# Kernel optimization log

Hardware: AMD Instinct MI355X
Metric: run time of the kernel (lower is better)

Reference implementation:

```python
import jax, jax.numpy as jnp
import numpy as np

B, T, D, H = 4, 2048, 1024, 16
HD = D // H  # 64
LOCAL_CTX, BLOCKSIZE, VERTSIZE = 256, 1, 16
STRIDE = LOCAL_CTX // BLOCKSIZE  # 256


def build_fixed_mask(n):
    # num_verts == 1 branch of generate_fixed_attention_mask
    layout = np.zeros((n, n), dtype=np.bool_)
    # vertical stripes: top `vertsize` indices of each stride block
    for idx in range(STRIDE - VERTSIZE, STRIDE):
        layout[:, idx::STRIDE] = True
    rows = np.arange(n)
    # local: each query attends to its own stride-block
    same_block = (rows[:, None] // STRIDE) == (rows[None, :] // STRIDE)
    layout |= same_block
    # causal: zero out k > q
    layout &= rows[None, :] <= rows[:, None]
    return layout


def setup_inputs() -> dict:
    key = jax.random.key(0)
    k1, k2, k3, k4, k5 = jax.random.split(key, 5)
    s = 0.02
    return {
        "x": jax.random.normal(k1, (B, T, D), dtype=jnp.float32),
        "Wqkv": jax.random.normal(k2, (D, 3 * D), dtype=jnp.float32) * s,
        "bqkv": jax.random.normal(k3, (3 * D,), dtype=jnp.float32) * s,
        "Wproj": jax.random.normal(k4, (D, D), dtype=jnp.float32) * s,
        "bproj": jax.random.normal(k5, (D,), dtype=jnp.float32) * s,
        "mask": jnp.asarray(build_fixed_mask(T)),
    }


def reference(x, Wqkv, bqkv, Wproj, bproj, mask):
    b, t, _ = x.shape
    qkv = (x @ Wqkv + bqkv).reshape(b, t, 3, H, HD)
    # (B,T,3,H,HD) -> (B,H,T,HD) per component
    q = qkv[:, :, 0].transpose(0, 2, 1, 3)
    k = qkv[:, :, 1].transpose(0, 2, 1, 3)
    v = qkv[:, :, 2].transpose(0, 2, 1, 3)
    att = jnp.einsum("bhqd,bhkd->bhqk", q, k) * (1.0 / jnp.sqrt(jnp.float32(HD)))
    att = jnp.where(mask[:t, :t], att, -jnp.inf)
    att = jax.nn.softmax(att, axis=-1)
    y = jnp.einsum("bhqk,bhkd->bhqd", att, v)
    y = y.transpose(0, 2, 1, 3).reshape(b, t, D)
    return y @ Wproj + bproj
```

## Files before the change

### kernel.cpp

```cpp
#include <hip/hip_runtime.h>
#include <cstdint>
#include <cstddef>

typedef unsigned short u16;
typedef __attribute__((ext_vector_type(8))) short short8;
typedef __attribute__((ext_vector_type(4))) float f32x4;
typedef __attribute__((ext_vector_type(4))) unsigned short u16x4;

#define B_ 4
#define T_ 2048
#define D_ 1024
#define H_ 16
#define HD_ 64

__device__ __forceinline__ u16 f2bf(float f) {
  union { float f; unsigned i; } v; v.f = f;
  unsigned r = (v.i + 0x7FFFu + ((v.i >> 16) & 1u)) >> 16;
  return (u16)r;
}

__device__ __forceinline__ void load_lds16(const void* g, void* l) {
  __builtin_amdgcn_global_load_lds(
      (const __attribute__((address_space(1))) void*)g,
      (__attribute__((address_space(3))) void*)l, 16, 0, 0);
}

#define BAR() __builtin_amdgcn_s_barrier()
#define VMC(n) asm volatile("s_waitcnt vmcnt(" #n ")" ::: "memory")

__global__ __launch_bounds__(256) void cvt_f32_bf16(const float* __restrict__ src,
                                                    u16* __restrict__ dst) {
  const size_t i = ((size_t)blockIdx.x * 256 + threadIdx.x) * 4;
  const f32x4 v = *(const f32x4*)(src + i);
  u16x4 o;
#pragma unroll
  for (int r = 0; r < 4; ++r) o[r] = f2bf(v[r]);
  *(u16x4*)(dst + i) = o;
}

__global__ __launch_bounds__(256) void transpose_cvt(const float* __restrict__ src,
                                                     u16* __restrict__ dst,
                                                     int R, int C) {
  __shared__ u16 t[32][33];
  const int c0 = blockIdx.x * 32, r0 = blockIdx.y * 32;
  const int tid = threadIdx.x;
  const int lr = tid >> 5, lc = tid & 31;
#pragma unroll
  for (int p = 0; p < 4; ++p)
    t[lr + p * 8][lc] = f2bf(src[(size_t)(r0 + lr + p * 8) * C + c0 + lc]);
  __syncthreads();
#pragma unroll
  for (int p = 0; p < 4; ++p)
    dst[(size_t)(c0 + lr + p * 8) * R + r0 + lc] = t[lc][lr + p * 8];
}

template <int EPI>
__global__ __launch_bounds__(512, 2)
void gemm8p(const u16* __restrict__ A, const u16* __restrict__ Bt,
            const float* __restrict__ bias, int K, int N,
            void* __restrict__ o0v, u16* __restrict__ o1, u16* __restrict__ o2) {
  __shared__ u16 tbuf[65536];
  const int tid = threadIdx.x;
  const int lane = tid & 63;
  const int w = tid >> 6;
  const int q = lane >> 4, col = lane & 15;

  const int nbx = gridDim.x;
  const int id = blockIdx.y * nbx + blockIdx.x;
  const int nwg = nbx * gridDim.y;
  const int sid = (id & 7) * (nwg >> 3) + (id >> 3);
  const int m0 = (sid / nbx) * 256, n0 = (sid % nbx) * 256;

  const int c8 = ((lane & 7) ^ (lane >> 3)) * 8;
  const size_t go0 = (size_t)(w * 16 + (lane >> 3)) * K + c8;
  const size_t go1 = (size_t)(w * 16 + 8 + (lane >> 3)) * K + c8;
  const int d0 = w * 1024 + lane * 8, d1 = d0 + 512;

  auto STAGE = [&](int isB, int buf, int half, int tile) {
    const u16* s = isB ? Bt : A;
    const u16* g = s + (size_t)((isB ? n0 : m0) + half * 128) * K + ((size_t)tile << 6);
    u16* d = tbuf + (isB ? 32768 : 0) + (buf * 2 + half) * 8192;
    load_lds16(g + go0, d + d0);
    load_lds16(g + go1, d + d1);
  };

  short8 af[4][2], bfr[2][2];
  const int arow = (w >> 2) * 64 + col;
  const int brow = (w & 3) * 32 + col;
  const int sA0 = ((0 * 4 + q) ^ (col & 7)) * 8, sA1 = ((1 * 4 + q) ^ (col & 7)) * 8;

  auto LDA = [&](int buf, int pm) {
    const u16* base = tbuf + (buf * 2 + pm) * 8192;
#pragma unroll
    for (int i = 0; i < 4; ++i) {
      af[i][0] = *(const short8*)&base[(arow + i * 16) * 64 + sA0];
      af[i][1] = *(const short8*)&base[(arow + i * 16) * 64 + sA1];
    }
  };
  auto LDB = [&](int buf, int pn) {
    const u16* base = tbuf + 32768 + (buf * 2 + pn) * 8192;
#pragma unroll
    for (int j = 0; j < 2; ++j) {
      bfr[j][0] = *(const short8*)&base[(brow + j * 16) * 64 + sA0];
      bfr[j][1] = *(const short8*)&base[(brow + j * 16) * 64 + sA1];
    }
  };

  f32x4 acc[8][4] = {};
  auto MM = [&](int pm, int pn) {
    __builtin_amdgcn_s_setprio(1);
#pragma unroll
    for (int i = 0; i < 4; ++i)
#pragma unroll
      for (int j = 0; j < 2; ++j) {
        acc[pm * 4 + i][pn * 2 + j] =
            __builtin_amdgcn_mfma_f32_16x16x32_bf16(af[i][0], bfr[j][0], acc[pm * 4 + i][pn * 2 + j], 0, 0, 0);
        acc[pm * 4 + i][pn * 2 + j] =
            __builtin_amdgcn_mfma_f32_16x16x32_bf16(af[i][1], bfr[j][1], acc[pm * 4 + i][pn * 2 + j], 0, 0, 0);
      }
    __builtin_amdgcn_s_setprio(0);
  };

  const int NI = K >> 7;

  STAGE(0, 0, 0, 0); STAGE(0, 0, 1, 0); STAGE(1, 0, 0, 0); STAGE(1, 0, 1, 0);
  STAGE(0, 1, 0, 1); STAGE(0, 1, 1, 1); STAGE(1, 1, 0, 1);
  VMC(0);
  BAR();

  for (int i = 0; i < NI; ++i) {
    const int t1 = 2 * i + 1, t2 = 2 * i + 2, t3 = 2 * i + 3;
    const bool pf = (i < NI - 1);
    LDA(0, 0); LDB(0, 0);
    STAGE(1, 1, 1, t1);
    BAR(); MM(0, 0); BAR();
    LDB(0, 1);
    if (pf) STAGE(0, 0, 0, t2);
    BAR(); MM(0, 1); BAR();
    LDA(0, 1); LDB(0, 0);
    BAR(); MM(1, 0); BAR();
    LDB(0, 1);
    if (pf) { STAGE(1, 0, 0, t2); STAGE(0, 0, 1, t2); }
    BAR(); MM(1, 1);
    if (pf) { VMC(6); } else { VMC(0); }
    BAR();
    LDA(1, 0); LDB(1, 0);
    if (pf) STAGE(1, 0, 1, t2);
    BAR(); MM(0, 0); BAR();
    LDB(1, 1);
    if (pf) STAGE(0, 1, 0, t3);
    BAR(); MM(0, 1); BAR();
    LDA(1, 1); LDB(1, 0);
    BAR(); MM(1, 0); BAR();
    LDB(1, 1);
    if (pf) { STAGE(1, 1, 0, t3); STAGE(0, 1, 1, t3); }
    BAR(); MM(1, 1);
    if (pf) { VMC(6); }
    BAR();
  }

#pragma unroll
  for (int bj = 0; bj < 4; ++bj) {
    const int n = n0 + (w & 3) * 32 + (bj >> 1) * 128 + (bj & 1) * 16 + col;
    const float bv = bias[n];
    if constexpr (EPI == 0) {
      u16* q0p = (u16*)o0v;
      const int c = n >> 10, rem = n & 1023, hh = rem >> 6, dd = rem & 63;
#pragma unroll
      for (int a = 0; a < 8; ++a) {
        const int mrow = m0 + (w >> 2) * 64 + (a >> 2) * 128 + (a & 3) * 16 + q * 4;
        const int b = mrow >> 11, t2r = mrow & 2047;
        const int bh = b * H_ + hh;
        if (c == 0) {
#pragma unroll
          for (int r = 0; r < 4; ++r)
            q0p[((size_t)bh * T_ + t2r + r) * HD_ + dd] = f2bf((acc[a][bj][r] + bv) * 0.125f);
        } else if (c == 1) {
#pragma unroll
          for (int r = 0; r < 4; ++r)
            o1[((size_t)bh * T_ + t2r + r) * HD_ + dd] = f2bf(acc[a][bj][r] + bv);
        } else {
          u16x4 pk;
#pragma unroll
          for (int r = 0; r < 4; ++r) pk[r] = f2bf(acc[a][bj][r] + bv);
          *(u16x4*)&o2[((size_t)bh * HD_ + dd) * T_ + t2r] = pk;
        }
      }
    } else {
      float* outp = (float*)o0v;
#pragma unroll
      for (int a = 0; a < 8; ++a) {
        const int mrow = m0 + (w >> 2) * 64 + (a >> 2) * 128 + (a & 3) * 16 + q * 4;
#pragma unroll
        for (int r = 0; r < 4; ++r)
          outp[(size_t)(mrow + r) * N + n] = acc[a][bj][r] + bv;
      }
    }
  }
}

template <int EPI>
__global__ __launch_bounds__(256)
void gemm_bt(const u16* __restrict__ A, const u16* __restrict__ Bt,
             const float* __restrict__ bias, int K, int N,
             void* __restrict__ o0v, u16* __restrict__ o1, u16* __restrict__ o2) {
  __shared__ u16 As[128 * 32];
  __shared__ u16 Bs[128 * 32];
  const int tid = threadIdx.x;
  const int lane = tid & 63;
  const int w = tid >> 6;
  const int q = lane >> 4, col = lane & 15;
  const int m0 = blockIdx.y * 128, n0 = blockIdx.x * 128;
  const int wm = (w >> 1) * 64, wn = (w & 1) * 64;
  const int srow = tid >> 2, soff = (tid & 3) * 8;

  f32x4 acc[4][4] = {};

  const u16* Ap = A + (size_t)(m0 + srow) * K + soff;
  const u16* Bp = Bt + (size_t)(n0 + srow) * K + soff;

  for (int kb = 0; kb < K; kb += 32) {
    load_lds16(Ap + kb, &As[tid * 8]);
    load_lds16(Ap + (size_t)64 * K + kb, &As[2048 + tid * 8]);
    load_lds16(Bp + kb, &Bs[tid * 8]);
    load_lds16(Bp + (size_t)64 * K + kb, &Bs[2048 + tid * 8]);
    __syncthreads();
    short8 af[4], bfr[4];
#pragma unroll
    for (int i = 0; i < 4; ++i)
      af[i] = *(const short8*)&As[(wm + i * 16 + col) * 32 + q * 8];
#pragma unroll
    for (int j = 0; j < 4; ++j)
      bfr[j] = *(const short8*)&Bs[(wn + j * 16 + col) * 32 + q * 8];
#pragma unroll
    for (int i = 0; i < 4; ++i)
#pragma unroll
      for (int j = 0; j < 4; ++j)
        acc[i][j] = __builtin_amdgcn_mfma_f32_16x16x32_bf16(af[i], bfr[j], acc[i][j], 0, 0, 0);
    __syncthreads();
  }

#pragma unroll
  for (int j = 0; j < 4; ++j) {
    const int n = n0 + wn + j * 16 + col;
    const float bv = bias[n];
    if constexpr (EPI == 0) {
      u16* q0p = (u16*)o0v;
      const int c = n >> 10, rem = n & 1023, hh = rem >> 6, dd = rem & 63;
#pragma unroll
      for (int i = 0; i < 4; ++i) {
        const int mrow = m0 + wm + i * 16 + q * 4;
        const int b = mrow >> 11, t = mrow & 2047;
        const int bh = b * H_ + hh;
        if (c == 0) {
#pragma unroll
          for (int r = 0; r < 4; ++r)
            q0p[((size_t)bh * T_ + t + r) * HD_ + dd] = f2bf((acc[i][j][r] + bv) * 0.125f);
        } else if (c == 1) {
#pragma unroll
          for (int r = 0; r < 4; ++r)
            o1[((size_t)bh * T_ + t + r) * HD_ + dd] = f2bf(acc[i][j][r] + bv);
        } else {
          u16x4 pk;
#pragma unroll
          for (int r = 0; r < 4; ++r) pk[r] = f2bf(acc[i][j][r] + bv);
          *(u16x4*)&o2[((size_t)bh * HD_ + dd) * T_ + t] = pk;
        }
      }
    } else {
      float* outp = (float*)o0v;
#pragma unroll
      for (int i = 0; i < 4; ++i) {
        const int mrow = m0 + wm + i * 16 + q * 4;
#pragma unroll
        for (int r = 0; r < 4; ++r)
          outp[(size_t)(mrow + r) * N + n] = acc[i][j][r] + bv;
      }
    }
  }
}

__global__ __launch_bounds__(256)
void sparse_attn(const u16* __restrict__ Qb, const u16* __restrict__ Kb,
                 const u16* __restrict__ Vt, u16* __restrict__ Y) {
  __shared__ char smem[20480];
  u16* Pall = (u16*)smem;
  float* Obuf = (float*)smem;

  const int tid = threadIdx.x, lane = tid & 63, w = tid >> 6;
  const int q = lane >> 4, col = lane & 15;
  const int bh = blockIdx.x, qt = blockIdx.y;
  const int b = bh >> 4, hh = bh & 15;
  const int qb = qt >> 2;
  const int rb = (qt & 3) * 64;
  const int qg = qt * 64;
  const u16* Qh = Qb + (size_t)bh * T_ * HD_;
  const u16* Kh = Kb + (size_t)bh * T_ * HD_;
  const u16* Vh = Vt + (size_t)bh * HD_ * T_;

  short8 qf[4][2];
#pragma unroll
  for (int i = 0; i < 4; ++i)
#pragma unroll
    for (int h2 = 0; h2 < 2; ++h2)
      qf[i][h2] = *(const short8*)&Qh[(size_t)(qg + i * 16 + col) * HD_ + h2 * 32 + q * 8];

  f32x4 o[4][4] = {};
  f32x4 lI[4] = {};
  const short8 ones = {0x3F80, 0x3F80, 0x3F80, 0x3F80, 0x3F80, 0x3F80, 0x3F80, 0x3F80};

  u16* P = Pall + w * 2560;

  const int ns = (qb + 1) >> 1;
  const int L = ns + 2 * (qt & 3) + 2;

  for (int j = w; j < L; j += 4) {
    int k0, k1, localc;
    bool mask1;
    if (j < ns) {
      k0 = (2 * j) * 256 + 240; k1 = k0 + 256;
      mask1 = (2 * j + 1 == qb); localc = -1;
    } else {
      const int c = j - ns;
      k0 = qb * 256 + c * 32; k1 = k0 + 16;
      mask1 = false; localc = c * 32;
    }
    short8 k0a = *(const short8*)&Kh[(size_t)(k0 + col) * HD_ + q * 8];
    short8 k0b = *(const short8*)&Kh[(size_t)(k0 + col) * HD_ + 32 + q * 8];
    short8 k1a = *(const short8*)&Kh[(size_t)(k1 + col) * HD_ + q * 8];
    short8 k1b = *(const short8*)&Kh[(size_t)(k1 + col) * HD_ + 32 + q * 8];
    const int kvb = (q < 2) ? (k0 + q * 8) : (k1 + (q - 2) * 8);
    short8 vf[4];
#pragma unroll
    for (int dt = 0; dt < 4; ++dt)
      vf[dt] = *(const short8*)&Vh[(size_t)(dt * 16 + col) * T_ + kvb];
#pragma unroll
    for (int rt = 0; rt < 4; ++rt) {
      f32x4 z = {0.f, 0.f, 0.f, 0.f};
      f32x4 s0 = __builtin_amdgcn_mfma_f32_16x16x32_bf16(qf[rt][0], k0a, z, 0, 0, 0);
      s0 = __builtin_amdgcn_mfma_f32_16x16x32_bf16(qf[rt][1], k0b, s0, 0, 0, 0);
      f32x4 s1 = __builtin_amdgcn_mfma_f32_16x16x32_bf16(qf[rt][0], k1a, z, 0, 0, 0);
      s1 = __builtin_amdgcn_mfma_f32_16x16x32_bf16(qf[rt][1], k1b, s1, 0, 0, 0);
#pragma unroll
      for (int r = 0; r < 4; ++r) {
        float p0 = __expf(s0[r]);
        float p1 = mask1 ? 0.f : __expf(s1[r]);
        if (localc >= 0) {
          const int qr = rb + rt * 16 + q * 4 + r;
          if (localc + col > qr) p0 = 0.f;
          if (localc + 16 + col > qr) p1 = 0.f;
        }
        P[(rt * 16 + q * 4 + r) * 40 + col] = f2bf(p0);
        P[(rt * 16 + q * 4 + r) * 40 + 16 + col] = f2bf(p1);
      }
    }
    asm volatile("s_waitcnt lgkmcnt(0)" ::: "memory");
    short8 pf[4];
#pragma unroll
    for (int rt = 0; rt < 4; ++rt)
      pf[rt] = *(const short8*)&P[(rt * 16 + col) * 40 + q * 8];
#pragma unroll
    for (int rt = 0; rt < 4; ++rt) {
#pragma unroll
      for (int dt = 0; dt < 4; ++dt)
        o[rt][dt] = __builtin_amdgcn_mfma_f32_16x16x32_bf16(pf[rt], vf[dt], o[rt][dt], 0, 0, 0);
      lI[rt] = __builtin_amdgcn_mfma_f32_16x16x32_bf16(pf[rt], ones, lI[rt], 0, 0, 0);
    }
  }

#pragma unroll
  for (int rt = 0; rt < 4; ++rt) {
    __syncthreads();
#pragma unroll
    for (int dt = 0; dt < 4; ++dt)
      *(f32x4*)&Obuf[(w * 65 + dt * 16 + col) * 16 + q * 4] = o[rt][dt];
    if (col == 0)
      *(f32x4*)&Obuf[(w * 65 + 64) * 16 + q * 4] = lI[rt];
    __syncthreads();
    f32x4 acc = {0.f, 0.f, 0.f, 0.f};
    f32x4 lt = {0.f, 0.f, 0.f, 0.f};
#pragma unroll
    for (int w2 = 0; w2 < 4; ++w2) {
      acc += *(const f32x4*)&Obuf[(w2 * 65 + w * 16 + col) * 16 + q * 4];
      lt += *(const f32x4*)&Obuf[(w2 * 65 + 64) * 16 + q * 4];
    }
#pragma unroll
    for (int r = 0; r < 4; ++r) {
      const int trow = qg + rt * 16 + q * 4 + r;
      Y[((size_t)(b * T_ + trow)) * D_ + hh * HD_ + w * 16 + col] = f2bf(acc[r] / lt[r]);
    }
  }
}

extern "C" void kernel_launch(void* const* d_in, const int* in_sizes, int n_in,
                              void* d_out, int out_size, void* d_ws, size_t ws_size,
                              hipStream_t stream) {
  const float* x = (const float*)d_in[0];
  const float* Wqkv = (const float*)d_in[1];
  const float* bqkv = (const float*)d_in[2];
  const float* Wproj = (const float*)d_in[3];
  const float* bproj = (const float*)d_in[4];
  float* out = (float*)d_out;

  char* ws = (char*)d_ws;
  u16* xb     = (u16*)(ws + 0);
  u16* WqkvT  = (u16*)(ws + 16777216);
  u16* WprojT = (u16*)(ws + 23068672);
  u16* Qb     = (u16*)(ws + 25165824);
  u16* Kb     = (u16*)(ws + 41943040);
  u16* Vt     = (u16*)(ws + 58720256);
  u16* Y      = (u16*)(ws + 75497472);

  cvt_f32_bf16<<<dim3(8192), 256, 0, stream>>>(x, xb);
  transpose_cvt<<<dim3(96, 32), 256, 0, stream>>>(Wqkv, WqkvT, 1024, 3072);
  transpose_cvt<<<dim3(32, 32), 256, 0, stream>>>(Wproj, WprojT, 1024, 1024);
  gemm8p<0><<<dim3(12, 32), 512, 0, stream>>>(xb, WqkvT, bqkv, 1024, 3072, Qb, Kb, Vt);
  sparse_attn<<<dim3(64, 32), 256, 0, stream>>>(Qb, Kb, Vt, Y);
  gemm_bt<1><<<dim3(8, 64), 256, 0, stream>>>(Y, WprojT, bproj, 1024, 1024, out, nullptr, nullptr);
}
```

Baseline: 258.9 us.

## Merge preprocessing kernels, swizzle proj GEMM tiles, prefetch K fragments in attention

Three unrelated changes. The x conversion and the two weight transposes now run as one launch, removing two kernel launches. The output-projection GEMM remaps workgroup IDs across eight groups to change L2 locality. The sparse attention loop software-prefetches the next iteration's K fragments so their latency overlaps the current MFMA and softmax work, at the cost of more registers.

Measured after the change: 254.7 us. No clear change (-1.6%).

```diff
diff --git a/kernel.cpp b/kernel.cpp
--- a/kernel.cpp
+++ b/kernel.cpp
@@ -28,22 +28,31 @@
 #define BAR() __builtin_amdgcn_s_barrier()
 #define VMC(n) asm volatile("s_waitcnt vmcnt(" #n ")" ::: "memory")
 
-__global__ __launch_bounds__(256) void cvt_f32_bf16(const float* __restrict__ src,
-                                                    u16* __restrict__ dst) {
-  const size_t i = ((size_t)blockIdx.x * 256 + threadIdx.x) * 4;
-  const f32x4 v = *(const f32x4*)(src + i);
-  u16x4 o;
-#pragma unroll
-  for (int r = 0; r < 4; ++r) o[r] = f2bf(v[r]);
-  *(u16x4*)(dst + i) = o;
-}
-
-__global__ __launch_bounds__(256) void transpose_cvt(const float* __restrict__ src,
-                                                     u16* __restrict__ dst,
-                                                     int R, int C) {
+__global__ __launch_bounds__(256)
+void pre_all(const float* __restrict__ x, u16* __restrict__ xb,
+             const float* __restrict__ Wqkv, u16* __restrict__ WqkvT,
+             const float* __restrict__ Wproj, u16* __restrict__ WprojT) {
   __shared__ u16 t[32][33];
-  const int c0 = blockIdx.x * 32, r0 = blockIdx.y * 32;
+  const int bid = blockIdx.x;
   const int tid = threadIdx.x;
+  if (bid < 8192) {
+    const size_t i = ((size_t)bid * 256 + tid) * 4;
+    const f32x4 v = *(const f32x4*)(x + i);
+    u16x4 o;
+#pragma unroll
+    for (int r = 0; r < 4; ++r) o[r] = f2bf(v[r]);
+    *(u16x4*)(xb + i) = o;
+    return;
+  }
+  const float* src; u16* dst; int R, C, bx, by;
+  if (bid < 11264) {
+    const int tb = bid - 8192;
+    bx = tb % 96; by = tb / 96; src = Wqkv; dst = WqkvT; R = 1024; C = 3072;
+  } else {
+    const int tb = bid - 11264;
+    bx = tb & 31; by = tb >> 5; src = Wproj; dst = WprojT; R = 1024; C = 1024;
+  }
+  const int c0 = bx * 32, r0 = by * 32;
   const int lr = tid >> 5, lc = tid & 31;
 #pragma unroll
   for (int p = 0; p < 4; ++p)
@@ -210,7 +219,13 @@
   const int lane = tid & 63;
   const int w = tid >> 6;
   const int q = lane >> 4, col = lane & 15;
-  const int m0 = blockIdx.y * 128, n0 = blockIdx.x * 128;
+
+  const int nbx = gridDim.x;
+  const int id = blockIdx.y * nbx + blockIdx.x;
+  const int nwg = nbx * gridDim.y;
+  const int sid = (id & 7) * (nwg >> 3) + (id >> 3);
+  const int m0 = (sid / nbx) * 128, n0 = (sid % nbx) * 128;
+
   const int wm = (w >> 1) * 64, wn = (w & 1) * 64;
   const int srow = tid >> 2, soff = (tid & 3) * 8;
 
@@ -314,9 +329,7 @@
   const int ns = (qb + 1) >> 1;
   const int L = ns + 2 * (qt & 3) + 2;
 
-  for (int j = w; j < L; j += 4) {
-    int k0, k1, localc;
-    bool mask1;
+  auto params = [&](int j, int& k0, int& k1, bool& mask1, int& localc) {
     if (j < ns) {
       k0 = (2 * j) * 256 + 240; k1 = k0 + 256;
       mask1 = (2 * j + 1 == qb); localc = -1;
@@ -325,22 +338,38 @@
       k0 = qb * 256 + c * 32; k1 = k0 + 16;
       mask1 = false; localc = c * 32;
     }
-    short8 k0a = *(const short8*)&Kh[(size_t)(k0 + col) * HD_ + q * 8];
-    short8 k0b = *(const short8*)&Kh[(size_t)(k0 + col) * HD_ + 32 + q * 8];
-    short8 k1a = *(const short8*)&Kh[(size_t)(k1 + col) * HD_ + q * 8];
-    short8 k1b = *(const short8*)&Kh[(size_t)(k1 + col) * HD_ + 32 + q * 8];
+  };
+  auto ldK = [&](int k0, int k1, short8* kf) {
+    kf[0] = *(const short8*)&Kh[(size_t)(k0 + col) * HD_ + q * 8];
+    kf[1] = *(const short8*)&Kh[(size_t)(k0 + col) * HD_ + 32 + q * 8];
+    kf[2] = *(const short8*)&Kh[(size_t)(k1 + col) * HD_ + q * 8];
+    kf[3] = *(const short8*)&Kh[(size_t)(k1 + col) * HD_ + 32 + q * 8];
+  };
+
+  int k0 = 0, k1 = 0, localc = -1;
+  bool mask1 = false;
+  short8 kf[4];
+  if (w < L) { params(w, k0, k1, mask1, localc); ldK(k0, k1, kf); }
+
+  for (int j = w; j < L; j += 4) {
     const int kvb = (q < 2) ? (k0 + q * 8) : (k1 + (q - 2) * 8);
     short8 vf[4];
 #pragma unroll
     for (int dt = 0; dt < 4; ++dt)
       vf[dt] = *(const short8*)&Vh[(size_t)(dt * 16 + col) * T_ + kvb];
+    int nk0 = 0, nk1 = 0, nlocalc = -1;
+    bool nmask1 = false;
+    short8 nkf[4];
+    const bool hn = (j + 4) < L;
+    if (hn) { params(j + 4, nk0, nk1, nmask1, nlocalc); ldK(nk0, nk1, nkf); }
+
 #pragma unroll
     for (int rt = 0; rt < 4; ++rt) {
       f32x4 z = {0.f, 0.f, 0.f, 0.f};
-      f32x4 s0 = __builtin_amdgcn_mfma_f32_16x16x32_bf16(qf[rt][0], k0a, z, 0, 0, 0);
-      s0 = __builtin_amdgcn_mfma_f32_16x16x32_bf16(qf[rt][1], k0b, s0, 0, 0, 0);
-      f32x4 s1 = __builtin_amdgcn_mfma_f32_16x16x32_bf16(qf[rt][0], k1a, z, 0, 0, 0);
-      s1 = __builtin_amdgcn_mfma_f32_16x16x32_bf16(qf[rt][1], k1b, s1, 0, 0, 0);
+      f32x4 s0 = __builtin_amdgcn_mfma_f32_16x16x32_bf16(qf[rt][0], kf[0], z, 0, 0, 0);
+      s0 = __builtin_amdgcn_mfma_f32_16x16x32_bf16(qf[rt][1], kf[1], s0, 0, 0, 0);
+      f32x4 s1 = __builtin_amdgcn_mfma_f32_16x16x32_bf16(qf[rt][0], kf[2], z, 0, 0, 0);
+      s1 = __builtin_amdgcn_mfma_f32_16x16x32_bf16(qf[rt][1], kf[3], s1, 0, 0, 0);
 #pragma unroll
       for (int r = 0; r < 4; ++r) {
         float p0 = __expf(s0[r]);
@@ -366,6 +395,10 @@
         o[rt][dt] = __builtin_amdgcn_mfma_f32_16x16x32_bf16(pf[rt], vf[dt], o[rt][dt], 0, 0, 0);
       lI[rt] = __builtin_amdgcn_mfma_f32_16x16x32_bf16(pf[rt], ones, lI[rt], 0, 0, 0);
     }
+    if (hn) {
+      k0 = nk0; k1 = nk1; mask1 = nmask1; localc = nlocalc;
+      kf[0] = nkf[0]; kf[1] = nkf[1]; kf[2] = nkf[2]; kf[3] = nkf[3];
+    }
   }
 
 #pragma unroll
@@ -411,9 +444,7 @@
   u16* Vt     = (u16*)(ws + 58720256);
   u16* Y      = (u16*)(ws + 75497472);
 
-  cvt_f32_bf16<<<dim3(8192), 256, 0, stream>>>(x, xb);
-  transpose_cvt<<<dim3(96, 32), 256, 0, stream>>>(Wqkv, WqkvT, 1024, 3072);
-  transpose_cvt<<<dim3(32, 32), 256, 0, stream>>>(Wproj, WprojT, 1024, 1024);
+  pre_all<<<dim3(12288), 256, 0, stream>>>(x, xb, Wqkv, WqkvT, Wproj, WprojT);
   gemm8p<0><<<dim3(12, 32), 512, 0, stream>>>(xb, WqkvT, bqkv, 1024, 3072, Qb, Kb, Vt);
   sparse_attn<<<dim3(64, 32), 256, 0, stream>>>(Qb, Kb, Vt, Y);
   gemm_bt<1><<<dim3(8, 64), 256, 0, stream>>>(Y, WprojT, bproj, 1024, 1024, out, nullptr, nullptr);
```
